# Kernel optimization log

Hardware: AMD Instinct MI355X
Metric: run time of the kernel (lower is better)

Reference implementation:

```python
import jax, jax.numpy as jnp
import numpy as np
import math

EMBED = 768
HEADS = 12
HEAD_DIM = EMBED // HEADS

def setup_inputs() -> dict:
    key = jax.random.key(0)
    ks = jax.random.split(key, 9)
    B, T, C = 32, 1024, EMBED
    s = 1.0 / math.sqrt(C)
    return {
        "hidden_states": jax.random.normal(ks[0], (B, T, C), dtype=jnp.float32),
        "q_w": jax.random.normal(ks[1], (C, C), dtype=jnp.float32) * s,
        "q_b": jnp.zeros((C,), dtype=jnp.float32),
        "k_w": jax.random.normal(ks[2], (C, C), dtype=jnp.float32) * s,
        "k_b": jnp.zeros((C,), dtype=jnp.float32),
        "v_w": jax.random.normal(ks[3], (C, C), dtype=jnp.float32) * s,
        "v_b": jnp.zeros((C,), dtype=jnp.float32),
        "o_w": jax.random.normal(ks[4], (C, C), dtype=jnp.float32) * s,
        "o_b": jnp.zeros((C,), dtype=jnp.float32),
    }

def reference(hidden_states, q_w, q_b, k_w, k_b, v_w, v_b, o_w, o_b):
    B, T, C = hidden_states.shape
    H, D = HEADS, C // HEADS
    # Linear: x @ W^T + b (torch nn.Linear convention); here weights stored (C, C)
    q = (hidden_states @ q_w.T + q_b).reshape(B, T, H, D).transpose(0, 2, 1, 3)
    k = (hidden_states @ k_w.T + k_b).reshape(B, T, H, D).transpose(0, 2, 1, 3)
    v = (hidden_states @ v_w.T + v_b).reshape(B, T, H, D).transpose(0, 2, 1, 3)
    scale = 1.0 / math.sqrt(D)
    scores = jnp.einsum("bhqd,bhkd->bhqk", q, k) * scale
    attn = jax.nn.softmax(scores, axis=-1)
    out = jnp.einsum("bhqk,bhkd->bhqd", attn, v)  # (B,H,T,D)
    out = out.transpose(0, 2, 1, 3).reshape(B, T, C)
    return out @ o_w.T + o_b
```

## Files before the change

### kernel.cpp

```cpp
#include <hip/hip_runtime.h>
#include <hip/hip_bf16.h>

#define B_ 32
#define T_ 1024
#define C_ 768
#define H_ 12
#define D_ 64
#define BT_ (B_*T_)
#define CC_ (C_*C_)

typedef __attribute__((ext_vector_type(4))) float f32x4;
typedef __attribute__((ext_vector_type(8))) short bf16x8;
typedef __attribute__((ext_vector_type(4))) short short4_t;
typedef unsigned short u16;
typedef unsigned int u32;

#define QSCALE 0.1803368801111244f

__device__ __forceinline__ float bf2f(u16 u){
  union { float f; unsigned int i; } v; v.i = ((unsigned int)u)<<16; return v.f;
}
__device__ __forceinline__ u16 f2bf(float f){
  union { float f; unsigned int i; } v; v.f = f;
  return (u16)((v.i + 0x7fffu + ((v.i>>16)&1u)) >> 16);
}
__device__ __forceinline__ u16 f2bf_fast(float f){
  union { float f; unsigned int i; } v; v.f = f;
  return (u16)((v.i + 0x8000u) >> 16);
}
__device__ __forceinline__ void split2(float f, u16& h, u16& l){
  h = f2bf(f);
  l = f2bf(f - bf2f(h));
}

__device__ __forceinline__ void gll16(const void* g, void* l){
  __builtin_amdgcn_global_load_lds(
      (const __attribute__((address_space(1))) u32*)g,
      (__attribute__((address_space(3))) u32*)l, 16, 0, 0);
}

__global__ void sentinel_kernel(float* out, int n){
  int i = blockIdx.x*blockDim.x + threadIdx.x;
  if (i < n) out[i] = 12345.0f;
}

__global__ void xquant_kernel(const float* __restrict__ x, u16* __restrict__ xb, int n8){
  int i = blockIdx.x*blockDim.x + threadIdx.x;
  int stride = gridDim.x*blockDim.x;
  for (; i < n8; i += stride) {
    f32x4 a = *(const f32x4*)(x + (size_t)i*8);
    f32x4 b = *(const f32x4*)(x + (size_t)i*8 + 4);
    bf16x8 o;
    #pragma unroll
    for (int j = 0; j < 4; ++j) { o[j] = (short)f2bf(a[j]); o[j+4] = (short)f2bf(b[j]); }
    *(bf16x8*)(xb + (size_t)i*8) = o;
  }
}

__global__ void wquant_kernel(const float* __restrict__ qw, const float* __restrict__ kw,
                              const float* __restrict__ vw, const float* __restrict__ ow,
                              u16* __restrict__ W3b, u16* __restrict__ Wohi,
                              u16* __restrict__ Wolo){
  int i = (blockIdx.x*blockDim.x + threadIdx.x)*4;
  if (i >= CC_) return;
  f32x4 q = *(const f32x4*)(qw+i);
  f32x4 k = *(const f32x4*)(kw+i);
  f32x4 v = *(const f32x4*)(vw+i);
  f32x4 o = *(const f32x4*)(ow+i);
  short4_t tq, tk, tv, th, tl;
  #pragma unroll
  for (int j = 0; j < 4; ++j) {
    tq[j] = (short)f2bf(q[j]);
    tk[j] = (short)f2bf(k[j]);
    tv[j] = (short)f2bf(v[j]);
    u16 hh, ll; split2(o[j], hh, ll);
    th[j] = (short)hh; tl[j] = (short)ll;
  }
  *(short4_t*)(W3b + i)          = tq;
  *(short4_t*)(W3b + CC_ + i)    = tk;
  *(short4_t*)(W3b + 2*CC_ + i)  = tv;
  *(short4_t*)(Wohi + i)         = th;
  *(short4_t*)(Wolo + i)         = tl;
}

template<int MODE>
__global__ __launch_bounds__(256,2)
void gemm_glds(const u16* __restrict__ Ab, const u16* __restrict__ Wb,
               const u16* __restrict__ Wlo_,
               const float* __restrict__ bq, const float* __restrict__ bk,
               const float* __restrict__ bv,
               u16* __restrict__ Qb, u16* __restrict__ Kb, u16* __restrict__ Vb,
               float* __restrict__ Out)
{
  __shared__ __align__(1024) u16 sA[128*64];
  __shared__ __align__(1024) u16 sB[128*64];
  __shared__ __align__(1024) u16 sBl[MODE==1 ? 128*64 : 8];
  const int tid = threadIdx.x;
  const int lane = tid & 63;
  const int l15 = lane & 15, l16 = lane >> 4;
  const int wave = tid >> 6;
  const int wr = wave >> 1, wc = wave & 1;

  const int bid = blockIdx.x;
  const int xcd = bid & 7;
  const int idx = bid >> 3;
  int z, nb, mloc;
  if (MODE == 0) { z = idx % 3; int r = idx / 3; nb = r % 6; mloc = r / 6; }
  else           { z = 0; nb = idx % 6; mloc = idx / 6; }
  const int m0 = (xcd*32 + mloc) * 128;
  const int n0 = nb * 128;
  const u16* W = (MODE==0) ? (Wb + (size_t)z*CC_) : Wb;
  const float* bias = (MODE==1) ? bq : (z==0 ? bq : (z==1 ? bk : bv));

  const int lrow = lane >> 3;
  const int cbyte = ((lane & 7) ^ lrow) << 4;

  f32x4 acc[4][4];
  #pragma unroll
  for (int i=0;i<4;++i)
    #pragma unroll
    for (int j=0;j<4;++j)
      acc[i][j] = (f32x4){0.f,0.f,0.f,0.f};

  for (int k0 = 0; k0 < C_; k0 += 64) {
    __syncthreads();
    #pragma unroll
    for (int sg = 0; sg < 4; ++sg) {
      int seg = wave*4 + sg;
      int row = seg*8 + lrow;
      gll16((const char*)(Ab + (size_t)(m0+row)*C_ + k0) + cbyte, sA + seg*512);
      gll16((const char*)(W  + (size_t)(n0+row)*C_ + k0) + cbyte, sB + seg*512);
      if (MODE == 1)
        gll16((const char*)(Wlo_ + (size_t)(n0+row)*C_ + k0) + cbyte, sBl + seg*512);
    }
    asm volatile("s_waitcnt vmcnt(0)" ::: "memory");
    __syncthreads();

    #pragma unroll
    for (int kc = 0; kc < 2; ++kc) {
      bf16x8 a[4], bh[4], bl[4];
      #pragma unroll
      for (int mf = 0; mf < 4; ++mf) {
        int row = wr*64 + mf*16 + l15;
        int off = (row<<7) + ((kc*64 + l16*16) ^ ((row&7)<<4));
        a[mf] = *(const bf16x8*)((const char*)sA + off);
      }
      #pragma unroll
      for (int nf = 0; nf < 4; ++nf) {
        int row = wc*64 + nf*16 + l15;
        int off = (row<<7) + ((kc*64 + l16*16) ^ ((row&7)<<4));
        bh[nf] = *(const bf16x8*)((const char*)sB + off);
        if (MODE == 1) bl[nf] = *(const bf16x8*)((const char*)sBl + off);
      }
      #pragma unroll
      for (int mf = 0; mf < 4; ++mf)
        #pragma unroll
        for (int nf = 0; nf < 4; ++nf) {
          acc[mf][nf] = __builtin_amdgcn_mfma_f32_16x16x32_bf16(a[mf], bh[nf], acc[mf][nf],0,0,0);
          if (MODE == 1)
            acc[mf][nf] = __builtin_amdgcn_mfma_f32_16x16x32_bf16(a[mf], bl[nf], acc[mf][nf],0,0,0);
        }
    }
  }

  #pragma unroll
  for (int mf = 0; mf < 4; ++mf) {
    #pragma unroll
    for (int nf = 0; nf < 4; ++nf) {
      int mgb = m0 + wr*64 + mf*16 + l16*4;
      int ng  = n0 + wc*64 + nf*16 + l15;
      float bv = bias[ng];
      if (MODE == 1) {
        #pragma unroll
        for (int r = 0; r < 4; ++r)
          Out[(size_t)(mgb+r)*C_ + ng] = acc[mf][nf][r] + bv;
      } else {
        int b = mgb >> 10, t0 = mgb & 1023;
        int h = ng >> 6, d = ng & 63;
        int bh_ = b*H_ + h;
        if (z == 2) {
          short4_t vh;
          #pragma unroll
          for (int r = 0; r < 4; ++r)
            vh[r] = (short)f2bf(acc[mf][nf][r] + bv);
          size_t idx2 = ((size_t)bh_*D_ + d)*T_ + t0;
          *(short4_t*)&Vb[idx2] = vh;
        } else {
          u16* dst = (z==0) ? Qb : Kb;
          float scale = (z==0) ? QSCALE : 1.0f;
          #pragma unroll
          for (int r = 0; r < 4; ++r) {
            size_t idx2 = ((size_t)bh_*T_ + (t0+r))*D_ + d;
            dst[idx2] = f2bf((acc[mf][nf][r] + bv) * scale);
          }
        }
      }
    }
  }
}

__global__ __launch_bounds__(256,2)
void attn_kernel(const u16* __restrict__ Qb, const u16* __restrict__ Kb,
                 const u16* __restrict__ Vb, u16* __restrict__ AOb)
{
  __shared__ __align__(16) u16 sK[64*64];
  __shared__ __align__(16) u16 sV[64*64];
  __shared__ __align__(16) u16 sP[4][32*64];
  const int tid = threadIdx.x;
  const int lane = tid & 63;
  const int l15 = lane & 15, l16 = lane >> 4;
  const int wave = tid >> 6;
  const int bid = blockIdx.x;
  const int sw  = (bid & 7) * 384 + (bid >> 3);
  const int bh  = sw >> 3;
  const int q0  = (sw & 7) * 128 + wave * 32;

  bf16x8 qh[2][2];
  #pragma unroll
  for (int mf = 0; mf < 2; ++mf)
    #pragma unroll
    for (int kc = 0; kc < 2; ++kc)
      qh[mf][kc] = *(const bf16x8*)(Qb + ((size_t)bh*T_ + q0 + mf*16 + l15)*D_ + kc*32 + l16*8);

  f32x4 o[2][4];
  #pragma unroll
  for (int mf = 0; mf < 2; ++mf)
    #pragma unroll
    for (int i = 0; i < 4; ++i) o[mf][i] = (f32x4){0.f,0.f,0.f,0.f};
  float l_r[2][4] = {{0.f,0.f,0.f,0.f},{0.f,0.f,0.f,0.f}};

  const size_t kbase = (size_t)bh * (T_*D_);
  const size_t vbase = (size_t)bh * (D_*T_);
  char* pb = (char*)sP[wave];

  int srow[2], sdst[2], scolb[2];
  #pragma unroll
  for (int iss = 0; iss < 2; ++iss) {
    int oo = (iss*256 + tid)*16;
    srow[iss]  = oo >> 7;
    scolb[iss] = oo & 127;
    sdst[iss]  = (srow[iss]<<7) | (scolb[iss] ^ ((srow[iss]&7)<<4));
  }
  bf16x8 kreg[2], vreg[2];
  #pragma unroll
  for (int iss = 0; iss < 2; ++iss) {
    kreg[iss] = *(const bf16x8*)((const char*)(Kb + kbase + (size_t)srow[iss]*D_) + scolb[iss]);
    vreg[iss] = *(const bf16x8*)((const char*)(Vb + vbase + (size_t)srow[iss]*T_) + scolb[iss]);
  }

  for (int kt = 0; kt < T_/64; ++kt) {
    __syncthreads();
    #pragma unroll
    for (int iss = 0; iss < 2; ++iss) {
      *(bf16x8*)((char*)sK + sdst[iss]) = kreg[iss];
      *(bf16x8*)((char*)sV + sdst[iss]) = vreg[iss];
    }
    if (kt + 1 < T_/64) {
      #pragma unroll
      for (int iss = 0; iss < 2; ++iss) {
        kreg[iss] = *(const bf16x8*)((const char*)(Kb + kbase + (size_t)((kt+1)*64+srow[iss])*D_) + scolb[iss]);
        vreg[iss] = *(const bf16x8*)((const char*)(Vb + vbase + (size_t)srow[iss]*T_ + (kt+1)*64) + scolb[iss]);
      }
    }
    __syncthreads();

    f32x4 s[2][4];
    #pragma unroll
    for (int mf = 0; mf < 2; ++mf)
      #pragma unroll
      for (int nf = 0; nf < 4; ++nf) s[mf][nf] = (f32x4){0.f,0.f,0.f,0.f};
    #pragma unroll
    for (int nf = 0; nf < 4; ++nf) {
      #pragma unroll
      for (int kc = 0; kc < 2; ++kc) {
        int row = nf*16 + l15;
        int off = (row<<7) | (((kc*64) + l16*16) ^ ((row&7)<<4));
        bf16x8 kf = *(const bf16x8*)((const char*)sK + off);
        s[0][nf] = __builtin_amdgcn_mfma_f32_16x16x32_bf16(qh[0][kc], kf, s[0][nf],0,0,0);
        s[1][nf] = __builtin_amdgcn_mfma_f32_16x16x32_bf16(qh[1][kc], kf, s[1][nf],0,0,0);
      }
    }

    #pragma unroll
    for (int mf = 0; mf < 2; ++mf)
      #pragma unroll
      for (int nf = 0; nf < 4; ++nf)
        #pragma unroll
        for (int r = 0; r < 4; ++r) {
          float p = __builtin_amdgcn_exp2f(s[mf][nf][r]);
          l_r[mf][r] += p;
          int qr = mf*16 + l16*4 + r;
          int off = (qr<<7) | (((nf*16 + l15)<<1) ^ ((qr&7)<<4));
          *(u16*)(pb + off) = f2bf_fast(p);
        }

    #pragma unroll
    for (int kc = 0; kc < 2; ++kc) {
      int offp0 = (l15<<7) | (((kc*64) + l16*16) ^ ((l15&7)<<4));
      int row1 = 16 + l15;
      int offp1 = (row1<<7) | (((kc*64) + l16*16) ^ ((row1&7)<<4));
      bf16x8 pa0 = *(const bf16x8*)(pb + offp0);
      bf16x8 pa1 = *(const bf16x8*)(pb + offp1);
      #pragma unroll
      for (int df = 0; df < 4; ++df) {
        int row = df*16 + l15;
        int offv = (row<<7) | (((kc*64) + l16*16) ^ ((row&7)<<4));
        bf16x8 vf = *(const bf16x8*)((const char*)sV + offv);
        o[0][df] = __builtin_amdgcn_mfma_f32_16x16x32_bf16(pa0, vf, o[0][df],0,0,0);
        o[1][df] = __builtin_amdgcn_mfma_f32_16x16x32_bf16(pa1, vf, o[1][df],0,0,0);
      }
    }
  }

  #pragma unroll
  for (int mf = 0; mf < 2; ++mf)
    #pragma unroll
    for (int r = 0; r < 4; ++r) {
      float t = l_r[mf][r];
      #pragma unroll
      for (int off = 1; off < 16; off <<= 1)
        t += __shfl_xor(t, off);
      l_r[mf][r] = t;
    }

  const int b = bh / H_, h = bh % H_;
  #pragma unroll
  for (int mf = 0; mf < 2; ++mf)
    #pragma unroll
    for (int r = 0; r < 4; ++r) {
      float inv = 1.0f / l_r[mf][r];
      int t = q0 + mf*16 + l16*4 + r;
      size_t rowb = ((size_t)(b*T_ + t))*C_ + h*D_;
      #pragma unroll
      for (int df = 0; df < 4; ++df)
        AOb[rowb + df*16 + l15] = f2bf(o[mf][df][r] * inv);
    }
}

extern "C" void kernel_launch(void* const* d_in, const int* in_sizes, int n_in,
                              void* d_out, int out_size, void* d_ws, size_t ws_size,
                              hipStream_t stream) {
  const float* X  = (const float*)d_in[0];
  const float* qw = (const float*)d_in[1];
  const float* qb = (const float*)d_in[2];
  const float* kw = (const float*)d_in[3];
  const float* kb = (const float*)d_in[4];
  const float* vw = (const float*)d_in[5];
  const float* vb = (const float*)d_in[6];
  const float* ow = (const float*)d_in[7];
  const float* ob = (const float*)d_in[8];
  float* out = (float*)d_out;

  const size_t SZ = (size_t)BT_*C_*sizeof(u16);
  const size_t NEED = 4*SZ + 5*(size_t)CC_*sizeof(u16);
  if (ws_size < NEED) {
    sentinel_kernel<<<(out_size+255)/256,256,0,stream>>>(out, out_size);
    return;
  }
  char* ws = (char*)d_ws;
  u16* Qb   = (u16*)(ws + 0*SZ);
  u16* Kb   = (u16*)(ws + 1*SZ);
  u16* Vb   = (u16*)(ws + 2*SZ);
  u16* AOb  = (u16*)(ws + 3*SZ);
  u16* W3b  = (u16*)(ws + 4*SZ);
  u16* Wohi = W3b + 3*(size_t)CC_;
  u16* Wolo = Wohi + (size_t)CC_;
  u16* Xb   = AOb;

  wquant_kernel<<<CC_/4/256,256,0,stream>>>(qw, kw, vw, ow, W3b, Wohi, Wolo);
  xquant_kernel<<<2048,256,0,stream>>>(X, Xb, BT_*C_/8);
  gemm_glds<0><<<4608,256,0,stream>>>(Xb, W3b, nullptr, qb, kb, vb,
      Qb, Kb, Vb, nullptr);
  attn_kernel<<<3072,256,0,stream>>>(Qb, Kb, Vb, AOb);
  gemm_glds<1><<<1536,256,0,stream>>>(AOb, Wohi, Wolo, ob, nullptr, nullptr,
      nullptr, nullptr, nullptr, out);
}
```

Before: 382.7 us.

## Compute transposed QK^T so P tiles pack into vectorized LDS writes

Swaps the MFMA operands in the score computation so each lane holds four consecutive key scores for a single query row. The probabilities can then be packed two per 32-bit word and written to LDS as 8-byte vector stores instead of 16 scalar u16 stores, with a matching swizzle on the read side. The row-sum bookkeeping shrinks to one accumulator per m-fragment, with a cheaper cross-lane reduction and a shuffle at the end to redistribute the sums. It also raises wave priority around the MFMA loops with s_setprio, which may change how waves interleave.

After: 362.3 us. 1.06x faster.

```diff
diff --git a/kernel.cpp b/kernel.cpp
--- a/kernel.cpp
+++ b/kernel.cpp
@@ -12,6 +12,7 @@
 typedef __attribute__((ext_vector_type(4))) float f32x4;
 typedef __attribute__((ext_vector_type(8))) short bf16x8;
 typedef __attribute__((ext_vector_type(4))) short short4_t;
+typedef __attribute__((ext_vector_type(2))) unsigned int u32x2;
 typedef unsigned short u16;
 typedef unsigned int u32;
 
@@ -24,9 +25,9 @@
   union { float f; unsigned int i; } v; v.f = f;
   return (u16)((v.i + 0x7fffu + ((v.i>>16)&1u)) >> 16);
 }
-__device__ __forceinline__ u16 f2bf_fast(float f){
-  union { float f; unsigned int i; } v; v.f = f;
-  return (u16)((v.i + 0x8000u) >> 16);
+__device__ __forceinline__ u32 pack2bf(float lo, float hi){
+  union { float f; u32 i; } a, b; a.f = lo; b.f = hi;
+  return ((a.i + 0x8000u) >> 16) | ((b.i + 0x8000u) & 0xFFFF0000u);
 }
 __device__ __forceinline__ void split2(float f, u16& h, u16& l){
   h = f2bf(f);
@@ -205,7 +206,7 @@
 {
   __shared__ __align__(16) u16 sK[64*64];
   __shared__ __align__(16) u16 sV[64*64];
-  __shared__ __align__(16) u16 sP[4][32*64];
+  __shared__ __align__(16) u32 sP[4][32*32];
   const int tid = threadIdx.x;
   const int lane = tid & 63;
   const int l15 = lane & 15, l16 = lane >> 4;
@@ -227,11 +228,11 @@
   for (int mf = 0; mf < 2; ++mf)
     #pragma unroll
     for (int i = 0; i < 4; ++i) o[mf][i] = (f32x4){0.f,0.f,0.f,0.f};
-  float l_r[2][4] = {{0.f,0.f,0.f,0.f},{0.f,0.f,0.f,0.f}};
+  float l_r[2] = {0.f, 0.f};
 
   const size_t kbase = (size_t)bh * (T_*D_);
   const size_t vbase = (size_t)bh * (D_*T_);
-  char* pb = (char*)sP[wave];
+  u32* pw = sP[wave];
 
   int srow[2], sdst[2], scolb[2];
   #pragma unroll
@@ -269,6 +270,7 @@
     for (int mf = 0; mf < 2; ++mf)
       #pragma unroll
       for (int nf = 0; nf < 4; ++nf) s[mf][nf] = (f32x4){0.f,0.f,0.f,0.f};
+    __builtin_amdgcn_s_setprio(1);
     #pragma unroll
     for (int nf = 0; nf < 4; ++nf) {
       #pragma unroll
@@ -276,59 +278,66 @@
         int row = nf*16 + l15;
         int off = (row<<7) | (((kc*64) + l16*16) ^ ((row&7)<<4));
         bf16x8 kf = *(const bf16x8*)((const char*)sK + off);
-        s[0][nf] = __builtin_amdgcn_mfma_f32_16x16x32_bf16(qh[0][kc], kf, s[0][nf],0,0,0);
-        s[1][nf] = __builtin_amdgcn_mfma_f32_16x16x32_bf16(qh[1][kc], kf, s[1][nf],0,0,0);
-      }
-    }
-
-    #pragma unroll
-    for (int mf = 0; mf < 2; ++mf)
-      #pragma unroll
-      for (int nf = 0; nf < 4; ++nf)
-        #pragma unroll
-        for (int r = 0; r < 4; ++r) {
-          float p = __builtin_amdgcn_exp2f(s[mf][nf][r]);
-          l_r[mf][r] += p;
-          int qr = mf*16 + l16*4 + r;
-          int off = (qr<<7) | (((nf*16 + l15)<<1) ^ ((qr&7)<<4));
-          *(u16*)(pb + off) = f2bf_fast(p);
-        }
-
+        s[0][nf] = __builtin_amdgcn_mfma_f32_16x16x32_bf16(kf, qh[0][kc], s[0][nf],0,0,0);
+        s[1][nf] = __builtin_amdgcn_mfma_f32_16x16x32_bf16(kf, qh[1][kc], s[1][nf],0,0,0);
+      }
+    }
+    __builtin_amdgcn_s_setprio(0);
+
+    #pragma unroll
+    for (int mf = 0; mf < 2; ++mf) {
+      int q = mf*16 + l15;
+      u32* prow = pw + q*32;
+      int swz = (q & 7) << 2;
+      #pragma unroll
+      for (int nf = 0; nf < 4; ++nf) {
+        float p0 = __builtin_amdgcn_exp2f(s[mf][nf][0]);
+        float p1 = __builtin_amdgcn_exp2f(s[mf][nf][1]);
+        float p2 = __builtin_amdgcn_exp2f(s[mf][nf][2]);
+        float p3 = __builtin_amdgcn_exp2f(s[mf][nf][3]);
+        l_r[mf] += (p0 + p1) + (p2 + p3);
+        u32x2 w2;
+        w2[0] = pack2bf(p0, p1);
+        w2[1] = pack2bf(p2, p3);
+        *(u32x2*)(prow + ((8*nf + 2*l16) ^ swz)) = w2;
+      }
+    }
+
+    __builtin_amdgcn_s_setprio(1);
     #pragma unroll
     for (int kc = 0; kc < 2; ++kc) {
-      int offp0 = (l15<<7) | (((kc*64) + l16*16) ^ ((l15&7)<<4));
-      int row1 = 16 + l15;
-      int offp1 = (row1<<7) | (((kc*64) + l16*16) ^ ((row1&7)<<4));
-      bf16x8 pa0 = *(const bf16x8*)(pb + offp0);
-      bf16x8 pa1 = *(const bf16x8*)(pb + offp1);
+      bf16x8 pf[2];
+      #pragma unroll
+      for (int mf = 0; mf < 2; ++mf) {
+        int q = mf*16 + l15;
+        pf[mf] = *(const bf16x8*)(pw + q*32 + ((kc*16 + l16*4) ^ ((q&7)<<2)));
+      }
       #pragma unroll
       for (int df = 0; df < 4; ++df) {
         int row = df*16 + l15;
         int offv = (row<<7) | (((kc*64) + l16*16) ^ ((row&7)<<4));
         bf16x8 vf = *(const bf16x8*)((const char*)sV + offv);
-        o[0][df] = __builtin_amdgcn_mfma_f32_16x16x32_bf16(pa0, vf, o[0][df],0,0,0);
-        o[1][df] = __builtin_amdgcn_mfma_f32_16x16x32_bf16(pa1, vf, o[1][df],0,0,0);
-      }
-    }
-  }
-
+        o[0][df] = __builtin_amdgcn_mfma_f32_16x16x32_bf16(pf[0], vf, o[0][df],0,0,0);
+        o[1][df] = __builtin_amdgcn_mfma_f32_16x16x32_bf16(pf[1], vf, o[1][df],0,0,0);
+      }
+    }
+    __builtin_amdgcn_s_setprio(0);
+  }
+
+  #pragma unroll
+  for (int mf = 0; mf < 2; ++mf) {
+    float t = l_r[mf];
+    t += __shfl_xor(t, 16);
+    t += __shfl_xor(t, 32);
+    l_r[mf] = t;
+  }
+
+  const int b = bh / H_, h = bh % H_;
   #pragma unroll
   for (int mf = 0; mf < 2; ++mf)
     #pragma unroll
     for (int r = 0; r < 4; ++r) {
-      float t = l_r[mf][r];
-      #pragma unroll
-      for (int off = 1; off < 16; off <<= 1)
-        t += __shfl_xor(t, off);
-      l_r[mf][r] = t;
-    }
-
-  const int b = bh / H_, h = bh % H_;
-  #pragma unroll
-  for (int mf = 0; mf < 2; ++mf)
-    #pragma unroll
-    for (int r = 0; r < 4; ++r) {
-      float inv = 1.0f / l_r[mf][r];
+      float inv = 1.0f / __shfl(l_r[mf], (l16 << 2) + r);
       int t = q0 + mf*16 + l16*4 + r;
       size_t rowb = ((size_t)(b*T_ + t))*C_ + h*D_;
       #pragma unroll
```
